# Kernel tuning notes

Hardware: AMD Instinct MI355X
Metric: run time of the kernel (lower is better)

## Reference

```python
import jax, jax.numpy as jnp
import numpy as np

THRESH = 0.5  # global `thresh` used by ActFun (NOT init_thresh)
LENS = 0.5    # global `lens` (surrogate window)
DECAY = 0.25  # init_decay


@jax.custom_vjp
def act_fun(u):
    return (u > THRESH).astype(u.dtype)

def _act_fwd(u):
    return act_fun(u), u

def _act_bwd(u, g):
    surrogate = (jnp.abs(u - THRESH) < LENS).astype(g.dtype) / (2.0 * LENS)
    return (g * surrogate,)

act_fun.defvjp(_act_fwd, _act_bwd)


def setup_inputs() -> dict:
    key = jax.random.key(0)
    x = jax.random.normal(key, (32, 256, 4096), dtype=jnp.float32)  # [T, B, D]
    return {"x": x}


def reference(x):
    # LIF recurrence: mem_t = mem_{t-1} * decay * (1 - stop_grad(spike_{t-1})) + x_t
    mem0 = x[0]
    spike0 = act_fun(mem0)

    def step(carry, x_t):
        mem, spike = carry
        mem = mem * DECAY * (1.0 - jax.lax.stop_gradient(spike)) + x_t
        s = act_fun(mem)
        return (mem, s), s

    _, spikes = jax.lax.scan(step, (mem0, spike0), x[1:])
    return jnp.concatenate([spike0[None], spikes], axis=0)  # [T, B, D]
```

## Files before the change

kernel.cpp:

```cpp
#include <hip/hip_runtime.h>


constexpr int   T_STEPS = 32;
constexpr int   CHUNK   = 8;
constexpr float THRESH  = 0.5f;
constexpr float DECAY   = 0.25f;

typedef float v4f __attribute__((ext_vector_type(4)));

__device__ __forceinline__ void load_chunk(float4* buf, const float4* __restrict__ xp,
                                           int t0, int n4) {
#pragma unroll
    for (int k = 0; k < CHUNK; ++k)
        buf[k] = xp[(t0 + k) * n4];
}

template <int T0>
__device__ __forceinline__ void compute_chunk(const float4* buf, float4& mem, float4& s,
                                              float4* __restrict__ op, int n4) {
#pragma unroll
    for (int k = 0; k < CHUNK; ++k) {
        float4 v = buf[k];
        if (T0 + k == 0) {
            mem = v;
        } else {
            mem.x = mem.x * (DECAY * (1.0f - s.x)) + v.x;
            mem.y = mem.y * (DECAY * (1.0f - s.y)) + v.y;
            mem.z = mem.z * (DECAY * (1.0f - s.z)) + v.z;
            mem.w = mem.w * (DECAY * (1.0f - s.w)) + v.w;
        }
        s.x = mem.x > THRESH ? 1.0f : 0.0f;
        s.y = mem.y > THRESH ? 1.0f : 0.0f;
        s.z = mem.z > THRESH ? 1.0f : 0.0f;
        s.w = mem.w > THRESH ? 1.0f : 0.0f;
        v4f sv = {s.x, s.y, s.z, s.w};
        __builtin_nontemporal_store(sv, (v4f*)(op + (T0 + k) * n4));
    }
}

__global__ __launch_bounds__(256) void lif_fwd_kernel(
    const float4* __restrict__ x,
    float4* __restrict__ out,
    int n4)
{
    int i = blockIdx.x * 256 + threadIdx.x;
    if (i >= n4) return;

    const float4* xp = x + i;
    float4*       op = out + i;

    float4 bufA[CHUNK], bufB[CHUNK];
    float4 mem, s;

    load_chunk(bufA, xp, 0, n4);
    load_chunk(bufB, xp, 8, n4);
    compute_chunk<0>(bufA, mem, s, op, n4);
    load_chunk(bufA, xp, 16, n4);
    compute_chunk<8>(bufB, mem, s, op, n4);
    load_chunk(bufB, xp, 24, n4);
    compute_chunk<16>(bufA, mem, s, op, n4);
    compute_chunk<24>(bufB, mem, s, op, n4);
}

extern "C" void kernel_launch(void* const* d_in, const int* in_sizes, int n_in,
                              void* d_out, int out_size, void* d_ws, size_t ws_size,
                              hipStream_t stream) {
    const float* x = (const float*)d_in[0];
    float* out = (float*)d_out;

    const int total = in_sizes[0];
    const int n     = total / T_STEPS;
    const int n4    = n / 4;

    const int block = 256;
    const int grid  = (n4 + block - 1) / block;

    lif_fwd_kernel<<<grid, block, 0, stream>>>(
        reinterpret_cast<const float4*>(x),
        reinterpret_cast<float4*>(out),
        n4);
}
```

Measured before the change: 232.8 us.

## Switch to float2 per thread with occupancy hint and compiler fences

Each thread now processes two elements instead of four, doubling the thread count and grid size so more waves are in flight to hide memory latency. It adds a launch-bounds minimum of 8 blocks per SM to cap register use, inserts compiler memory fences between pipeline stages to keep loads issued early, and uses 64-bit index arithmetic. The trade-off is narrower 8-byte memory transactions per lane and more per-thread overhead.

```diff
diff --git a/kernel.cpp b/kernel.cpp
--- a/kernel.cpp
+++ b/kernel.cpp
@@ -6,60 +6,64 @@
 constexpr float THRESH  = 0.5f;
 constexpr float DECAY   = 0.25f;
 
-typedef float v4f __attribute__((ext_vector_type(4)));
+typedef float v2f __attribute__((ext_vector_type(2)));
 
-__device__ __forceinline__ void load_chunk(float4* buf, const float4* __restrict__ xp,
-                                           int t0, int n4) {
+#define PIPELINE_FENCE() asm volatile("" ::: "memory")
+
+__device__ __forceinline__ void load_chunk(float2* buf, const float2* __restrict__ xp,
+                                           int t0, int n2) {
 #pragma unroll
     for (int k = 0; k < CHUNK; ++k)
-        buf[k] = xp[(t0 + k) * n4];
+        buf[k] = xp[(size_t)(t0 + k) * (size_t)n2];
 }
 
 template <int T0>
-__device__ __forceinline__ void compute_chunk(const float4* buf, float4& mem, float4& s,
-                                              float4* __restrict__ op, int n4) {
+__device__ __forceinline__ void compute_chunk(const float2* buf, float2& mem, float2& s,
+                                              float2* __restrict__ op, int n2) {
 #pragma unroll
     for (int k = 0; k < CHUNK; ++k) {
-        float4 v = buf[k];
+        float2 v = buf[k];
         if (T0 + k == 0) {
             mem = v;
         } else {
             mem.x = mem.x * (DECAY * (1.0f - s.x)) + v.x;
             mem.y = mem.y * (DECAY * (1.0f - s.y)) + v.y;
-            mem.z = mem.z * (DECAY * (1.0f - s.z)) + v.z;
-            mem.w = mem.w * (DECAY * (1.0f - s.w)) + v.w;
         }
         s.x = mem.x > THRESH ? 1.0f : 0.0f;
         s.y = mem.y > THRESH ? 1.0f : 0.0f;
-        s.z = mem.z > THRESH ? 1.0f : 0.0f;
-        s.w = mem.w > THRESH ? 1.0f : 0.0f;
-        v4f sv = {s.x, s.y, s.z, s.w};
-        __builtin_nontemporal_store(sv, (v4f*)(op + (T0 + k) * n4));
+        v2f sv = {s.x, s.y};
+        __builtin_nontemporal_store(sv, (v2f*)(op + (size_t)(T0 + k) * (size_t)n2));
     }
 }
 
-__global__ __launch_bounds__(256) void lif_fwd_kernel(
-    const float4* __restrict__ x,
-    float4* __restrict__ out,
-    int n4)
+__global__ __launch_bounds__(256, 8) void lif_fwd_kernel(
+    const float2* __restrict__ x,
+    float2* __restrict__ out,
+    int n2)
 {
     int i = blockIdx.x * 256 + threadIdx.x;
-    if (i >= n4) return;
+    if (i >= n2) return;
 
-    const float4* xp = x + i;
-    float4*       op = out + i;
+    const float2* xp = x + i;
+    float2*       op = out + i;
 
-    float4 bufA[CHUNK], bufB[CHUNK];
-    float4 mem, s;
+    float2 bufA[CHUNK], bufB[CHUNK];
+    float2 mem, s;
 
-    load_chunk(bufA, xp, 0, n4);
-    load_chunk(bufB, xp, 8, n4);
-    compute_chunk<0>(bufA, mem, s, op, n4);
-    load_chunk(bufA, xp, 16, n4);
-    compute_chunk<8>(bufB, mem, s, op, n4);
-    load_chunk(bufB, xp, 24, n4);
-    compute_chunk<16>(bufA, mem, s, op, n4);
-    compute_chunk<24>(bufB, mem, s, op, n4);
+    load_chunk(bufA, xp, 0, n2);
+    load_chunk(bufB, xp, 8, n2);
+    PIPELINE_FENCE();
+
+    compute_chunk<0>(bufA, mem, s, op, n2);
+    load_chunk(bufA, xp, 16, n2);
+    PIPELINE_FENCE();
+
+    compute_chunk<8>(bufB, mem, s, op, n2);
+    load_chunk(bufB, xp, 24, n2);
+    PIPELINE_FENCE();
+
+    compute_chunk<16>(bufA, mem, s, op, n2);
+    compute_chunk<24>(bufB, mem, s, op, n2);
 }
 
 extern "C" void kernel_launch(void* const* d_in, const int* in_sizes, int n_in,
@@ -70,13 +74,13 @@
 
     const int total = in_sizes[0];
     const int n     = total / T_STEPS;
-    const int n4    = n / 4;
+    const int n2    = n / 2;
 
     const int block = 256;
-    const int grid  = (n4 + block - 1) / block;
+    const int grid  = (n2 + block - 1) / block;
 
     lif_fwd_kernel<<<grid, block, 0, stream>>>(
-        reinterpret_cast<const float4*>(x),
-        reinterpret_cast<float4*>(out),
-        n4);
+        reinterpret_cast<const float2*>(x),
+        reinterpret_cast<float2*>(out),
+        n2);
 }
```

Result: slower. 239.1 us (+2.7%).

## Software-pipeline loads with inline asm waits and defer spike stores via bitmasks

Applied to the files above, without the earlier changes.

Replaces the chunked double-buffer with a rolling 8-deep load window issued via inline asm with exact s_waitcnt vmcnt values, so each timestep waits only for its own load. Spikes are accumulated as per-lane bitmasks and the decay factor is computed directly from the predicate. All output stores are emitted after the recurrence. This aims to keep memory loads continuously in flight, at the cost of bursty writes at the end and reliance on hand-written asm scheduling.

```diff
diff --git a/kernel.cpp b/kernel.cpp
--- a/kernel.cpp
+++ b/kernel.cpp
@@ -1,42 +1,58 @@
 #include <hip/hip_runtime.h>
+#include <stdint.h>
 
 
 constexpr int   T_STEPS = 32;
-constexpr int   CHUNK   = 8;
+constexpr int   DEPTH   = 8;
 constexpr float THRESH  = 0.5f;
 constexpr float DECAY   = 0.25f;
 
 typedef float v4f __attribute__((ext_vector_type(4)));
 
-__device__ __forceinline__ void load_chunk(float4* buf, const float4* __restrict__ xp,
-                                           int t0, int n4) {
-#pragma unroll
-    for (int k = 0; k < CHUNK; ++k)
-        buf[k] = xp[(t0 + k) * n4];
-}
+#define ISSUE(t)                                                         \
+    do {                                                                 \
+        const float4* _a = xp + (size_t)(t) * (size_t)n4;                \
+        asm volatile("global_load_dwordx4 %0, %1, off"                   \
+                     : "=&v"(buf[(t) % DEPTH])                           \
+                     : "v"(_a)                                           \
+                     : "memory");                                        \
+    } while (0)
 
-template <int T0>
-__device__ __forceinline__ void compute_chunk(const float4* buf, float4& mem, float4& s,
-                                              float4* __restrict__ op, int n4) {
-#pragma unroll
-    for (int k = 0; k < CHUNK; ++k) {
-        float4 v = buf[k];
-        if (T0 + k == 0) {
-            mem = v;
-        } else {
-            mem.x = mem.x * (DECAY * (1.0f - s.x)) + v.x;
-            mem.y = mem.y * (DECAY * (1.0f - s.y)) + v.y;
-            mem.z = mem.z * (DECAY * (1.0f - s.z)) + v.z;
-            mem.w = mem.w * (DECAY * (1.0f - s.w)) + v.w;
-        }
-        s.x = mem.x > THRESH ? 1.0f : 0.0f;
-        s.y = mem.y > THRESH ? 1.0f : 0.0f;
-        s.z = mem.z > THRESH ? 1.0f : 0.0f;
-        s.w = mem.w > THRESH ? 1.0f : 0.0f;
-        v4f sv = {s.x, s.y, s.z, s.w};
-        __builtin_nontemporal_store(sv, (v4f*)(op + (T0 + k) * n4));
-    }
-}
+#define WAITN(t)                                                         \
+    asm volatile("s_waitcnt vmcnt(%1)"                                   \
+                 : "+v"(buf[(t) % DEPTH])                                \
+                 : "n"(((DEPTH - 1) < (T_STEPS - 1 - (t)))               \
+                           ? (DEPTH - 1)                                 \
+                           : (T_STEPS - 1 - (t)))                        \
+                 : "memory");                                            \
+    __builtin_amdgcn_sched_barrier(0)
+
+#define STEP(t)                                                          \
+    do {                                                                 \
+        WAITN(t);                                                        \
+        v4f v = buf[(t) % DEPTH];                                        \
+        if ((t) == 0) {                                                  \
+            mem.x = v.x; mem.y = v.y; mem.z = v.z; mem.w = v.w;          \
+        } else {                                                         \
+            mem.x = mem.x * c.x + v.x;                                   \
+            mem.y = mem.y * c.y + v.y;                                   \
+            mem.z = mem.z * c.z + v.z;                                   \
+            mem.w = mem.w * c.w + v.w;                                   \
+        }                                                                \
+        bool px = mem.x > THRESH;                                        \
+        bool py = mem.y > THRESH;                                        \
+        bool pz = mem.z > THRESH;                                        \
+        bool pw = mem.w > THRESH;                                        \
+        bx |= px ? (1u << (t)) : 0u;                                     \
+        by |= py ? (1u << (t)) : 0u;                                     \
+        bz |= pz ? (1u << (t)) : 0u;                                     \
+        bw |= pw ? (1u << (t)) : 0u;                                     \
+        c.x = px ? 0.0f : DECAY;                                         \
+        c.y = py ? 0.0f : DECAY;                                         \
+        c.z = pz ? 0.0f : DECAY;                                         \
+        c.w = pw ? 0.0f : DECAY;                                         \
+        if ((t) + DEPTH < T_STEPS) ISSUE((t) + DEPTH);                   \
+    } while (0)
 
 __global__ __launch_bounds__(256) void lif_fwd_kernel(
     const float4* __restrict__ x,
@@ -49,17 +65,32 @@
     const float4* xp = x + i;
     float4*       op = out + i;
 
-    float4 bufA[CHUNK], bufB[CHUNK];
-    float4 mem, s;
+    v4f buf[DEPTH];
+    float4 mem = {0.f, 0.f, 0.f, 0.f};
+    float4 c   = {DECAY, DECAY, DECAY, DECAY};
+    uint32_t bx = 0, by = 0, bz = 0, bw = 0;
 
-    load_chunk(bufA, xp, 0, n4);
-    load_chunk(bufB, xp, 8, n4);
-    compute_chunk<0>(bufA, mem, s, op, n4);
-    load_chunk(bufA, xp, 16, n4);
-    compute_chunk<8>(bufB, mem, s, op, n4);
-    load_chunk(bufB, xp, 24, n4);
-    compute_chunk<16>(bufA, mem, s, op, n4);
-    compute_chunk<24>(bufB, mem, s, op, n4);
+    ISSUE(0); ISSUE(1); ISSUE(2); ISSUE(3);
+    ISSUE(4); ISSUE(5); ISSUE(6); ISSUE(7);
+
+    STEP(0);  STEP(1);  STEP(2);  STEP(3);
+    STEP(4);  STEP(5);  STEP(6);  STEP(7);
+    STEP(8);  STEP(9);  STEP(10); STEP(11);
+    STEP(12); STEP(13); STEP(14); STEP(15);
+    STEP(16); STEP(17); STEP(18); STEP(19);
+    STEP(20); STEP(21); STEP(22); STEP(23);
+    STEP(24); STEP(25); STEP(26); STEP(27);
+    STEP(28); STEP(29); STEP(30); STEP(31);
+
+#pragma unroll
+    for (int t = 0; t < T_STEPS; ++t) {
+        v4f sv;
+        sv.x = ((bx >> t) & 1u) ? 1.0f : 0.0f;
+        sv.y = ((by >> t) & 1u) ? 1.0f : 0.0f;
+        sv.z = ((bz >> t) & 1u) ? 1.0f : 0.0f;
+        sv.w = ((bw >> t) & 1u) ? 1.0f : 0.0f;
+        __builtin_nontemporal_store(sv, (v4f*)(op + (size_t)t * (size_t)n4));
+    }
 }
 
 extern "C" void kernel_launch(void* const* d_in, const int* in_sizes, int n_in,
```

Result: slower. 239.9 us (+3.0%).
